# Optimization experiments

Measured on AMD Instinct MI355X. Metric: run time of the kernel, lower is better.

Reference implementation:

```python
import jax, jax.numpy as jnp
import numpy as np
import math

DIM = 96
D_MODEL = 2 * DIM
EXPAND = 2
D_INNER = EXPAND * D_MODEL  # 384
D_STATE = 16
D_CONV = 3
DT_RANK = math.ceil(D_MODEL / 16)  # 12
K = 4
B, H, W = 2, 56, 56


def setup_inputs() -> dict:
    key = jax.random.key(0)
    ks = jax.random.split(key, 10)
    s = lambda k, shp, sc=0.02: jax.random.normal(k, shp, jnp.float32) * sc
    inp = {}
    inp["x"] = jax.random.normal(ks[0], (B, DIM, H, W), jnp.float32)
    inp["conv_init_w"] = s(ks[1], (2 * DIM, DIM))
    inp["conv_init_b"] = jnp.zeros((2 * DIM,), jnp.float32)
    inp["in_proj_w"] = s(ks[2], (2 * D_INNER, D_MODEL))
    inp["conv2d_w"] = s(ks[3], (D_INNER, 1, D_CONV, D_CONV), 0.1)
    inp["conv2d_b"] = jnp.zeros((D_INNER,), jnp.float32)
    inp["x_proj_w"] = s(ks[4], (K, DT_RANK + 2 * D_STATE, D_INNER))
    inp["dt_proj_w"] = s(ks[5], (K, D_INNER, DT_RANK), 0.1)
    inp["dt_proj_b"] = s(ks[6], (K, D_INNER), 0.1)
    A = jnp.tile(jnp.arange(1, D_STATE + 1, dtype=jnp.float32), (K, D_INNER, 1))
    inp["A_log"] = jnp.log(A)  # (K, d_inner, d_state)
    inp["Ds"] = jnp.ones((K, D_INNER), jnp.float32)
    inp["ln_g"] = jnp.ones((D_INNER,), jnp.float32)
    inp["ln_b"] = jnp.zeros((D_INNER,), jnp.float32)
    inp["out_proj_w"] = s(ks[7], (D_MODEL, D_INNER))
    inp["conv_fina_w"] = s(ks[8], (DIM, 2 * DIM))
    inp["conv_fina_b"] = jnp.zeros((DIM,), jnp.float32)
    return inp


def _gelu(x):
    return jax.nn.gelu(x, approximate=False)


def _silu(x):
    return x * jax.nn.sigmoid(x)


def _selective_scan(u, delta, A, Bs, Cs, D):
    # u, delta: (b,K,d,L); A: (K,d,N); Bs,Cs: (b,K,N,L); D: (K,d)
    b, k, d, L = u.shape
    N = A.shape[-1]

    def step(hst, inp):
        u_t, dl_t, B_t, C_t = inp  # (b,K,d),(b,K,d),(b,K,N),(b,K,N)
        hst = jnp.exp(dl_t[..., None] * A) * hst + (dl_t * u_t)[..., None] * B_t[:, :, None, :]
        y = jnp.einsum('bkdn,bkn->bkd', hst, C_t)
        return hst, y

    seq = (jnp.moveaxis(u, -1, 0), jnp.moveaxis(delta, -1, 0),
           jnp.moveaxis(Bs, -1, 0), jnp.moveaxis(Cs, -1, 0))
    h0 = jnp.zeros((b, k, d, N), u.dtype)
    _, ys = jax.lax.scan(step, h0, seq)
    y = jnp.moveaxis(ys, 0, -1)  # (b,K,d,L)
    return y + u * D[None, :, :, None]


def reference(x, conv_init_w, conv_init_b, in_proj_w, conv2d_w, conv2d_b,
              x_proj_w, dt_proj_w, dt_proj_b, A_log, Ds, ln_g, ln_b,
              out_proj_w, conv_fina_w, conv_fina_b):
    b, c, h, w = x.shape
    # conv_init: 1x1 conv + GELU (dim -> 2*dim)
    x1 = _gelu(jnp.einsum('bchw,oc->bohw', x, conv_init_w) + conv_init_b[None, :, None, None])
    x0 = x1
    xh = jnp.transpose(x1, (0, 2, 3, 1))  # b h w c
    # --- SS2D ---
    xz = xh @ in_proj_w.T  # (b,h,w,2*d_inner)
    xi, z = jnp.split(xz, 2, axis=-1)
    xi = jnp.transpose(xi, (0, 3, 1, 2))  # b d h w
    xi = jax.lax.conv_general_dilated(xi, conv2d_w, (1, 1), 'SAME',
                                      dimension_numbers=('NCHW', 'OIHW', 'NCHW'),
                                      feature_group_count=xi.shape[1])
    xi = _silu(xi + conv2d_b[None, :, None, None])
    d = xi.shape[1]
    L = h * w
    x_flat = xi.reshape(b, d, L)
    x_tr = jnp.transpose(xi, (0, 1, 3, 2)).reshape(b, d, L)  # column-major scan
    xs = jnp.stack([x_flat, x_tr], axis=1)                   # (b,2,d,L)
    xs = jnp.concatenate([xs, jnp.flip(xs, axis=-1)], 1)     # (b,4,d,L)
    x_dbl = jnp.einsum('bkdl,kcd->bkcl', xs, x_proj_w)
    dts = x_dbl[:, :, :DT_RANK]
    Bs = x_dbl[:, :, DT_RANK:DT_RANK + D_STATE]
    Cs = x_dbl[:, :, DT_RANK + D_STATE:]
    dts = jnp.einsum('bkrl,kdr->bkdl', dts, dt_proj_w)
    delta = jax.nn.softplus(dts + dt_proj_b[None, :, :, None])
    A = -jnp.exp(A_log)  # (K,d,N)
    out_y = _selective_scan(xs, delta, A, Bs, Cs, Ds)  # (b,4,d,L)
    inv_y = jnp.flip(out_y[:, 2:4], axis=-1)
    y1 = out_y[:, 0]
    y2 = inv_y[:, 0]
    wb = lambda t: jnp.transpose(t.reshape(b, d, w, h), (0, 1, 3, 2)).reshape(b, d, L)
    y3 = wb(out_y[:, 1])
    y4 = wb(inv_y[:, 1])
    y = y1 + y2 + y3 + y4  # (b,d,L)
    y = jnp.transpose(y, (0, 2, 1)).reshape(b, h, w, d)
    mu = y.mean(-1, keepdims=True)
    var = ((y - mu) ** 2).mean(-1, keepdims=True)
    y = (y - mu) * jax.lax.rsqrt(var + 1e-5) * ln_g + ln_b
    y = y * _silu(z)
    y = y @ out_proj_w.T  # (b,h,w,d_model)
    y = jnp.transpose(y, (0, 3, 1, 2))  # b c h w
    # residual add with x0, then conv_fina 1x1 + GELU
    out = _gelu(jnp.einsum('bchw,oc->bohw', y + x0, conv_fina_w) + conv_fina_b[None, :, None, None])
    return out
```

## Files before the change

kernel.cpp:

```cpp
#include <hip/hip_runtime.h>


#define LPIX 3136
#define HH 56
#define SEG 32
#define SEGLEN 98

__device__ __forceinline__ float gelu_f(float x) {
    return 0.5f * x * (1.0f + erff(x * 0.70710678118654752f));
}

__device__ __forceinline__ float quad_sum(float p) {
    p += __int_as_float(__builtin_amdgcn_update_dpp(0, __float_as_int(p), 0xB1, 0xf, 0xf, true));
    p += __int_as_float(__builtin_amdgcn_update_dpp(0, __float_as_int(p), 0x4E, 0xf, 0xf, true));
    return p;
}

template <int MODE>
__global__ __launch_bounds__(256) void gemm_k(
    const float* __restrict__ A, const float* __restrict__ A2,
    const float* __restrict__ W, const float* __restrict__ bias,
    float* __restrict__ out0, float* __restrict__ out1,
    int M, int N, int Kd)
{
    __shared__ __align__(16) float As[32][68];
    __shared__ __align__(16) float Ws[32][68];
    const int tid = threadIdx.x;
    const int m0 = blockIdx.x * 64;
    const int n0 = blockIdx.y * 64;
    const int kz = blockIdx.z;
    const int mi = tid >> 4, ni = tid & 15;
    const float* Ause = A;
    if constexpr (MODE == 4) {
        if (kz & 1) Ause = A2;
        W += (size_t)kz * 44 * Kd;
    }
    float acc[4][4] = {};

    for (int k0 = 0; k0 < Kd; k0 += 32) {
        #pragma unroll
        for (int p = 0; p < 2; ++p) {
            int r = (tid >> 3) + p * 32;
            int kv = (tid & 7) * 4;
            int m = m0 + r;
            float4 v;
            if constexpr (MODE == 3) {
                int b = m / LPIX, l = m % LPIX;
                const float* px = Ause + ((size_t)(b * 96 + k0 + kv)) * LPIX + l;
                v.x = px[0]; v.y = px[LPIX]; v.z = px[2 * LPIX]; v.w = px[3 * LPIX];
            } else {
                v = *reinterpret_cast<const float4*>(Ause + (size_t)m * Kd + k0 + kv);
                if constexpr (MODE == 2) {
                    float4 r2 = *reinterpret_cast<const float4*>(A2 + (size_t)m * Kd + k0 + kv);
                    v.x += r2.x; v.y += r2.y; v.z += r2.z; v.w += r2.w;
                }
            }
            As[kv + 0][r] = v.x; As[kv + 1][r] = v.y;
            As[kv + 2][r] = v.z; As[kv + 3][r] = v.w;
        }
        #pragma unroll
        for (int p = 0; p < 2; ++p) {
            int r = (tid >> 3) + p * 32;
            int kv = (tid & 7) * 4;
            int n = n0 + r;
            float4 v = make_float4(0.f, 0.f, 0.f, 0.f);
            if (n < N) v = *reinterpret_cast<const float4*>(W + (size_t)n * Kd + k0 + kv);
            Ws[kv + 0][r] = v.x; Ws[kv + 1][r] = v.y;
            Ws[kv + 2][r] = v.z; Ws[kv + 3][r] = v.w;
        }
        __syncthreads();
        #pragma unroll
        for (int kk = 0; kk < 32; ++kk) {
            float4 a = *reinterpret_cast<const float4*>(&As[kk][mi * 4]);
            float4 b = *reinterpret_cast<const float4*>(&Ws[kk][ni * 4]);
            float av[4] = {a.x, a.y, a.z, a.w};
            float bv[4] = {b.x, b.y, b.z, b.w};
            #pragma unroll
            for (int i = 0; i < 4; ++i)
                #pragma unroll
                for (int j = 0; j < 4; ++j)
                    acc[i][j] = fmaf(av[i], bv[j], acc[i][j]);
        }
        __syncthreads();
    }

    #pragma unroll
    for (int i = 0; i < 4; ++i) {
        int m = m0 + mi * 4 + i;
        int b = m / LPIX, l = m % LPIX;
        #pragma unroll
        for (int j = 0; j < 4; ++j) {
            int o = n0 + ni * 4 + j;
            float v = acc[i][j];
            if constexpr (MODE == 0) {
                if (o < 384) out0[((size_t)(b * 384 + o)) * LPIX + l] = v;
                else         out1[(size_t)m * 384 + (o - 384)] = v;
            } else if constexpr (MODE == 1) {
                out0[(size_t)m * N + o] = v;
            } else if constexpr (MODE == 2) {
                if (o < N) out0[((size_t)(b * 96 + o)) * LPIX + l] = gelu_f(v + bias[o]);
            } else if constexpr (MODE == 3) {
                out0[(size_t)m * N + o] = gelu_f(v + bias[o]);
            } else {
                if (o < 44)
                    out0[(((size_t)b * 4 + kz) * LPIX + l) * 48 + o] = v;
            }
        }
    }
}

__global__ __launch_bounds__(256) void dwconv_k(
    const float* __restrict__ xin, const float* __restrict__ w9,
    const float* __restrict__ bias, float* __restrict__ xout)
{
    int f = blockIdx.x * 256 + threadIdx.x;
    if (f >= LPIX) return;
    int c = blockIdx.y, b = blockIdx.z;
    const float* p = xin + ((size_t)b * 384 + c) * LPIX;
    int h = f / HH, w = f % HH;
    float s = bias[c];
    #pragma unroll
    for (int dh = -1; dh <= 1; ++dh) {
        int h2 = h + dh;
        if ((unsigned)h2 >= HH) continue;
        #pragma unroll
        for (int dw = -1; dw <= 1; ++dw) {
            int w2 = w + dw;
            if ((unsigned)w2 >= HH) continue;
            s = fmaf(p[h2 * HH + w2], w9[c * 9 + (dh + 1) * 3 + (dw + 1)], s);
        }
    }
    xout[((size_t)b * 384 + c) * LPIX + f] = s / (1.f + __expf(-s));
}

__global__ __launch_bounds__(256) void transR_k(
    const float* __restrict__ xi, const float* __restrict__ Ds,
    float* __restrict__ xiR, float* __restrict__ y0)
{
    __shared__ float T[64][65];
    int f0 = blockIdx.x * 64, d0 = blockIdx.y * 64, b = blockIdx.z;
    int tid = threadIdx.x;
    #pragma unroll
    for (int i = 0; i < 16; ++i) {
        int idx = tid + i * 256;
        int dl = idx >> 6, fl = idx & 63;
        T[dl][fl] = xi[((size_t)b * 384 + d0 + dl) * LPIX + f0 + fl];
    }
    __syncthreads();
    #pragma unroll
    for (int i = 0; i < 16; ++i) {
        int idx = tid + i * 256;
        int fl = idx >> 6, dl = idx & 63;
        int d = d0 + dl;
        float v = T[dl][fl];
        float sD = Ds[d] + Ds[384 + d] + Ds[768 + d] + Ds[1152 + d];
        size_t o = ((size_t)b * LPIX + f0 + fl) * 384 + d;
        xiR[o] = v;
        y0[o] = v * sD;
    }
}

__global__ __launch_bounds__(256) void transT_k(
    const float* __restrict__ xi, float* __restrict__ xiT)
{
    __shared__ float T[64][57];
    int d0 = blockIdx.x * 64, h = blockIdx.y, b = blockIdx.z;
    int tid = threadIdx.x;
    #pragma unroll
    for (int i = 0; i < 14; ++i) {
        int idx = tid + i * 256;
        int dl = idx / 56, wl = idx % 56;
        T[dl][wl] = xi[((size_t)b * 384 + d0 + dl) * LPIX + h * 56 + wl];
    }
    __syncthreads();
    #pragma unroll
    for (int i = 0; i < 14; ++i) {
        int idx = tid + i * 256;
        int wl = idx >> 6, dl = idx & 63;
        xiT[((size_t)b * LPIX + wl * 56 + h) * 384 + d0 + dl] = T[dl][wl];
    }
}

__global__ __launch_bounds__(256) void dtgemm_k(
    const float* __restrict__ xdblT, const float* __restrict__ dtw,
    const float* __restrict__ dtb, float* __restrict__ dT)
{
    __shared__ float As[64][13];
    __shared__ float Ws[64][13];
    int t0 = blockIdx.x * 64, d0 = blockIdx.y * 64;
    int bk = blockIdx.z, k = bk & 3;
    int tid = threadIdx.x;
    const float* Ab = xdblT + ((size_t)bk * LPIX + t0) * 48;
    for (int i = tid; i < 768; i += 256) {
        int tt = i / 12, r = i % 12;
        As[tt][r] = Ab[(size_t)tt * 48 + r];
    }
    for (int i = tid; i < 768; i += 256) {
        int dd = i / 12, r = i % 12;
        Ws[dd][r] = dtw[((size_t)k * 384 + d0 + dd) * 12 + r];
    }
    __syncthreads();
    int mi = tid >> 4, ni = tid & 15;
    float acc[4][4] = {};
    #pragma unroll
    for (int r = 0; r < 12; ++r) {
        float av[4], bv[4];
        #pragma unroll
        for (int i = 0; i < 4; ++i) av[i] = As[mi * 4 + i][r];
        #pragma unroll
        for (int j = 0; j < 4; ++j) bv[j] = Ws[ni * 4 + j][r];
        #pragma unroll
        for (int i = 0; i < 4; ++i)
            #pragma unroll
            for (int j = 0; j < 4; ++j)
                acc[i][j] = fmaf(av[i], bv[j], acc[i][j]);
    }
    #pragma unroll
    for (int i = 0; i < 4; ++i) {
        int t = t0 + mi * 4 + i;
        #pragma unroll
        for (int j = 0; j < 4; ++j) {
            int d = d0 + ni * 4 + j;
            float s = acc[i][j] + dtb[k * 384 + d];
            s = (s > 20.f) ? s : log1pf(__expf(s));
            dT[((size_t)bk * LPIX + t) * 384 + d] = s;
        }
    }
}

__global__ __launch_bounds__(256) void scan1_k(
    const float* __restrict__ dT, const float* __restrict__ xiR,
    const float* __restrict__ xiT, const float* __restrict__ xdblT,
    const float* __restrict__ A_log, float* __restrict__ lh,
    float* __restrict__ sumd)
{
    int w = blockIdx.x * 4 + (threadIdx.x >> 6);
    int lane = threadIdx.x & 63;
    int dl_ = lane >> 2, nq = lane & 3;
    int seg = w & (SEG - 1);
    int dblk = (w >> 5) % 24;
    int bk = w / (SEG * 24);
    int b = bk >> 2, k = bk & 3;
    int d = dblk * 16 + dl_;

    float4 Ar = *reinterpret_cast<const float4*>(A_log + ((size_t)(k * 384 + d)) * 16 + nq * 4);
    float A2[4] = { -__expf(Ar.x) * 1.44269504f, -__expf(Ar.y) * 1.44269504f,
                    -__expf(Ar.z) * 1.44269504f, -__expf(Ar.w) * 1.44269504f };

    const float* pD = dT + (size_t)bk * LPIX * 384;
    const float* pU = ((k & 1) ? xiT : xiR) + (size_t)b * LPIX * 384;
    const float* pBC = xdblT + (size_t)bk * LPIX * 48;

    int t0 = seg * SEGLEN;
    int rev = k >> 1;
    int fpos0 = rev ? (LPIX - 1 - t0) : t0;
    int stepd = rev ? -384 : 384;
    int stepbc = rev ? -48 : 48;

    unsigned idx = (unsigned)fpos0 * 384u + (unsigned)d;
    unsigned ibc = (unsigned)fpos0 * 48u + 12u + (unsigned)nq * 4u;

    float h0 = 0.f, h1 = 0.f, h2 = 0.f, h3 = 0.f, sd = 0.f;

    float dlv = pD[idx], uv = pU[idx];
    float4 Bv = *reinterpret_cast<const float4*>(pBC + ibc);
    for (int s = 0; s < SEGLEN; ++s) {
        float dln, un; float4 Bn;
        if (s < SEGLEN - 1) {
            idx += stepd; ibc += stepbc;
            dln = pD[idx]; un = pU[idx];
            Bn = *reinterpret_cast<const float4*>(pBC + ibc);
        }
        sd += dlv;
        float dlu = dlv * uv;
        h0 = fmaf(__builtin_amdgcn_exp2f(dlv * A2[0]), h0, dlu * Bv.x);
        h1 = fmaf(__builtin_amdgcn_exp2f(dlv * A2[1]), h1, dlu * Bv.y);
        h2 = fmaf(__builtin_amdgcn_exp2f(dlv * A2[2]), h2, dlu * Bv.z);
        h3 = fmaf(__builtin_amdgcn_exp2f(dlv * A2[3]), h3, dlu * Bv.w);
        dlv = dln; uv = un; Bv = Bn;
    }
    size_t hb = (((size_t)seg * 8 + bk) * 384 + d) * 16 + nq * 4;
    *reinterpret_cast<float4*>(lh + hb) = make_float4(h0, h1, h2, h3);
    if (nq == 0)
        sumd[((size_t)seg * 8 + bk) * 384 + d] = sd;
}

__global__ __launch_bounds__(256) void scan2_k(
    float* __restrict__ lh, const float* __restrict__ sumd,
    const float* __restrict__ A_log)
{
    int idx = blockIdx.x * 256 + threadIdx.x;
    int n = idx & 15;
    int d = (idx >> 4) % 384;
    int bk = idx / (384 * 16);
    int k = bk & 3;
    float A2 = -__expf(A_log[((size_t)(k * 384 + d)) * 16 + n]) * 1.44269504f;
    float h = 0.f;
    for (int s = 0; s < SEG; ++s) {
        size_t base = (((size_t)s * 8 + bk) * 384 + d) * 16 + n;
        float lhv = lh[base];
        float P = __builtin_amdgcn_exp2f(sumd[((size_t)s * 8 + bk) * 384 + d] * A2);
        lh[base] = h;
        h = fmaf(P, h, lhv);
    }
}

template <int KK, int REV>
__device__ __forceinline__ void scan3_body(
    int b, int bk, int k, int seg, int d, int nq, int lane,
    const float* __restrict__ dT, const float* __restrict__ pU,
    const float* __restrict__ xdblT, const float* __restrict__ A_log,
    const float* __restrict__ lh, float* __restrict__ y0)
{
    float4 Ar = *reinterpret_cast<const float4*>(A_log + ((size_t)(k * 384 + d)) * 16 + nq * 4);
    float A2[4] = { -__expf(Ar.x) * 1.44269504f, -__expf(Ar.y) * 1.44269504f,
                    -__expf(Ar.z) * 1.44269504f, -__expf(Ar.w) * 1.44269504f };

    const float* pD = dT + (size_t)bk * LPIX * 384;
    const float* pBC = xdblT + (size_t)bk * LPIX * 48;
    float* pY = y0 + (size_t)b * LPIX * 384;

    int t0 = seg * SEGLEN;
    int fpos0 = REV ? (LPIX - 1 - t0) : t0;
    constexpr int stepd = REV ? -384 : 384;
    constexpr int stepbc = REV ? -48 : 48;

    unsigned idx = (unsigned)fpos0 * 384u + (unsigned)d;
    unsigned ibc = (unsigned)fpos0 * 48u + 12u + (unsigned)nq * 4u;

    unsigned iy; int rr;
    if constexpr (KK) {
        int r0 = fpos0 % 56, q0 = fpos0 / 56;
        rr = r0;
        iy = (unsigned)(r0 * 56 + q0) * 384u + (unsigned)d;
    } else {
        iy = idx;
        rr = 0; (void)rr;
    }

    size_t hb = (((size_t)seg * 8 + bk) * 384 + d) * 16 + nq * 4;
    float4 h4 = *reinterpret_cast<const float4*>(lh + hb);
    float h0 = h4.x, h1 = h4.y, h2 = h4.z, h3 = h4.w;

    float dlv = pD[idx], uv = pU[idx];
    float4 Bv = *reinterpret_cast<const float4*>(pBC + ibc);
    float4 Cv = *reinterpret_cast<const float4*>(pBC + ibc + 16);

    for (int s = 0; s < SEGLEN; ++s) {
        float dln, un; float4 Bn, Cn;
        if (s < SEGLEN - 1) {
            idx += stepd; ibc += stepbc;
            dln = pD[idx]; un = pU[idx];
            Bn = *reinterpret_cast<const float4*>(pBC + ibc);
            Cn = *reinterpret_cast<const float4*>(pBC + ibc + 16);
        }
        float dlu = dlv * uv;
        h0 = fmaf(__builtin_amdgcn_exp2f(dlv * A2[0]), h0, dlu * Bv.x);
        float p = h0 * Cv.x;
        h1 = fmaf(__builtin_amdgcn_exp2f(dlv * A2[1]), h1, dlu * Bv.y);
        p = fmaf(h1, Cv.y, p);
        h2 = fmaf(__builtin_amdgcn_exp2f(dlv * A2[2]), h2, dlu * Bv.z);
        p = fmaf(h2, Cv.z, p);
        h3 = fmaf(__builtin_amdgcn_exp2f(dlv * A2[3]), h3, dlu * Bv.w);
        p = fmaf(h3, Cv.w, p);
        p = quad_sum(p);
        if ((lane & 3) == 0)
            __hip_atomic_fetch_add(pY + iy, p,
                                   __ATOMIC_RELAXED, __HIP_MEMORY_SCOPE_AGENT);
        if constexpr (KK) {
            if constexpr (REV) {
                bool wrap = (rr == 0);
                iy += wrap ? (unsigned)(3079 * 384) : (unsigned)(-56 * 384);
                rr = wrap ? 55 : rr - 1;
            } else {
                bool wrap = (rr == 55);
                iy += wrap ? (unsigned)(-3079 * 384) : (unsigned)(56 * 384);
                rr = wrap ? 0 : rr + 1;
            }
        } else {
            iy += (unsigned)stepd;
        }
        dlv = dln; uv = un; Bv = Bn; Cv = Cn;
    }
}

__global__ __launch_bounds__(256) void scan3_k(
    const float* __restrict__ dT, const float* __restrict__ xiR,
    const float* __restrict__ xiT, const float* __restrict__ xdblT,
    const float* __restrict__ A_log, const float* __restrict__ lh,
    float* __restrict__ y0)
{
    int w = blockIdx.x * 4 + (threadIdx.x >> 6);
    int lane = threadIdx.x & 63;
    int dl_ = lane >> 2, nq = lane & 3;
    int seg = w & (SEG - 1);
    int dblk = (w >> 5) % 24;
    int bk = w / (SEG * 24);
    int b = bk >> 2, k = bk & 3;
    int d = dblk * 16 + dl_;
    const float* pU = ((k & 1) ? xiT : xiR) + (size_t)b * LPIX * 384;
    if (k == 0)      scan3_body<0, 0>(b, bk, k, seg, d, nq, lane, dT, pU, xdblT, A_log, lh, y0);
    else if (k == 1) scan3_body<1, 0>(b, bk, k, seg, d, nq, lane, dT, pU, xdblT, A_log, lh, y0);
    else if (k == 2) scan3_body<0, 1>(b, bk, k, seg, d, nq, lane, dT, pU, xdblT, A_log, lh, y0);
    else             scan3_body<1, 1>(b, bk, k, seg, d, nq, lane, dT, pU, xdblT, A_log, lh, y0);
}

__global__ __launch_bounds__(256) void lngate_k(
    const float* __restrict__ y0, const float* __restrict__ z,
    const float* __restrict__ lng, const float* __restrict__ lnb,
    float* __restrict__ gbuf)
{
    int m = blockIdx.x * 4 + (threadIdx.x >> 6);
    int lane = threadIdx.x & 63;
    const float* py = y0 + (size_t)m * 384;
    float v[6];
    float s = 0.f, sq = 0.f;
    #pragma unroll
    for (int i = 0; i < 6; ++i) {
        v[i] = py[lane + i * 64];
        s += v[i]; sq += v[i] * v[i];
    }
    #pragma unroll
    for (int off = 1; off < 64; off <<= 1) {
        s += __shfl_xor(s, off);
        sq += __shfl_xor(sq, off);
    }
    float mu = s * (1.f / 384.f);
    float var = sq * (1.f / 384.f) - mu * mu;
    float rs = rsqrtf(var + 1e-5f);
    const float* pz = z + (size_t)m * 384;
    float* pg = gbuf + (size_t)m * 384;
    #pragma unroll
    for (int i = 0; i < 6; ++i) {
        int c = lane + i * 64;
        float nv = (v[i] - mu) * rs * lng[c] + lnb[c];
        float zv = pz[c];
        pg[c] = nv * (zv / (1.f + __expf(-zv)));
    }
}

extern "C" void kernel_launch(void* const* d_in, const int* in_sizes, int n_in,
                              void* d_out, int out_size, void* d_ws, size_t ws_size,
                              hipStream_t stream) {
    const float* x        = (const float*)d_in[0];
    const float* w_init   = (const float*)d_in[1];
    const float* b_init   = (const float*)d_in[2];
    const float* w_inproj = (const float*)d_in[3];
    const float* w_conv   = (const float*)d_in[4];
    const float* b_conv   = (const float*)d_in[5];
    const float* w_xproj  = (const float*)d_in[6];
    const float* w_dt     = (const float*)d_in[7];
    const float* b_dt     = (const float*)d_in[8];
    const float* A_log    = (const float*)d_in[9];
    const float* Ds       = (const float*)d_in[10];
    const float* ln_g     = (const float*)d_in[11];
    const float* ln_b     = (const float*)d_in[12];
    const float* w_out    = (const float*)d_in[13];
    const float* w_fina   = (const float*)d_in[14];
    const float* b_fina   = (const float*)d_in[15];

    float* ws    = (float*)d_ws;
    float* x1    = ws + 0;
    float* z     = ws + 1204224;
    float* xiR   = ws + 3612672;
    float* xiT   = ws + 6021120;
    float* xdblT = ws + 8429568;
    float* dT    = ws + 9633792;
    float* xiraw = ws + 9633792;
    float* xi    = ws + 12042240;
    float* y0    = ws + 19267584;
    float* lh    = ws + 21676032;
    float* sumd  = ws + 23248896;
    float* out   = (float*)d_out;

    gemm_k<3><<<dim3(98, 3), 256, 0, stream>>>(x, nullptr, w_init, b_init,
                                               x1, nullptr, 6272, 192, 96);
    gemm_k<0><<<dim3(98, 12), 256, 0, stream>>>(x1, nullptr, w_inproj, nullptr,
                                                xiraw, z, 6272, 768, 192);
    dwconv_k<<<dim3(13, 384, 2), 256, 0, stream>>>(xiraw, w_conv, b_conv, xi);
    transR_k<<<dim3(49, 6, 2), 256, 0, stream>>>(xi, Ds, xiR, y0);
    transT_k<<<dim3(6, 56, 2), 256, 0, stream>>>(xi, xiT);
    gemm_k<4><<<dim3(98, 1, 4), 256, 0, stream>>>(xiR, xiT, w_xproj, nullptr,
                                                  xdblT, nullptr, 6272, 44, 384);
    dtgemm_k<<<dim3(49, 6, 8), 256, 0, stream>>>(xdblT, w_dt, b_dt, dT);
    scan1_k<<<1536, 256, 0, stream>>>(dT, xiR, xiT, xdblT, A_log, lh, sumd);
    scan2_k<<<192, 256, 0, stream>>>(lh, sumd, A_log);
    scan3_k<<<1536, 256, 0, stream>>>(dT, xiR, xiT, xdblT, A_log, lh, y0);
    lngate_k<<<1568, 256, 0, stream>>>(y0, z, ln_g, ln_b, xiR);
    gemm_k<1><<<dim3(98, 3), 256, 0, stream>>>(xiR, nullptr, w_out, nullptr,
                                               dT, nullptr, 6272, 192, 384);
    gemm_k<2><<<dim3(98, 2), 256, 0, stream>>>(dT, x1, w_fina, b_fina,
                                               out, nullptr, 6272, 96, 192);
}
```

Before: 399.7 us.

## Fuse dwconv with transposes, add 128-row GEMM tiles, rebalance scan segments

The depthwise conv + SiLU now reads the channel-last in_proj output straight from a shared-memory tile and writes xiR, xiT and the D-skip term in one pass, replacing three kernels (dwconv, transR, transT). The in_proj, x_proj and out_proj GEMMs move to a 128-row tile variant with vectorised row-major stores, and the init GEMM loads its channel-major input with vector loads. The scan now uses 49 segments of 64 steps instead of 32 of 98, which gives more parallel blocks at the cost of a longer serial carry pass in scan2. The workspace layout is reshuffled so buffers can alias.

```diff
diff --git a/kernel.cpp b/kernel.cpp
--- a/kernel.cpp
+++ b/kernel.cpp
@@ -3,8 +3,9 @@
 
 #define LPIX 3136
 #define HH 56
-#define SEG 32
-#define SEGLEN 98
+#define SEG 49
+#define SEGLEN 64
+#define LOG2E 1.44269504f
 
 __device__ __forceinline__ float gelu_f(float x) {
     return 0.5f * x * (1.0f + erff(x * 0.70710678118654752f));
@@ -16,47 +17,38 @@
     return p;
 }
 
-template <int MODE>
+template <int AM, int EM>
 __global__ __launch_bounds__(256) void gemm_k(
     const float* __restrict__ A, const float* __restrict__ A2,
     const float* __restrict__ W, const float* __restrict__ bias,
-    float* __restrict__ out0, float* __restrict__ out1,
-    int M, int N, int Kd)
+    float* __restrict__ out0, int M, int N, int Kd)
 {
     __shared__ __align__(16) float As[32][68];
     __shared__ __align__(16) float Ws[32][68];
     const int tid = threadIdx.x;
     const int m0 = blockIdx.x * 64;
     const int n0 = blockIdx.y * 64;
-    const int kz = blockIdx.z;
     const int mi = tid >> 4, ni = tid & 15;
-    const float* Ause = A;
-    if constexpr (MODE == 4) {
-        if (kz & 1) Ause = A2;
-        W += (size_t)kz * 44 * Kd;
-    }
+    const int bI = m0 / LPIX, l0 = m0 % LPIX;
     float acc[4][4] = {};
 
     for (int k0 = 0; k0 < Kd; k0 += 32) {
-        #pragma unroll
-        for (int p = 0; p < 2; ++p) {
-            int r = (tid >> 3) + p * 32;
-            int kv = (tid & 7) * 4;
-            int m = m0 + r;
-            float4 v;
-            if constexpr (MODE == 3) {
-                int b = m / LPIX, l = m % LPIX;
-                const float* px = Ause + ((size_t)(b * 96 + k0 + kv)) * LPIX + l;
-                v.x = px[0]; v.y = px[LPIX]; v.z = px[2 * LPIX]; v.w = px[3 * LPIX];
-            } else {
-                v = *reinterpret_cast<const float4*>(Ause + (size_t)m * Kd + k0 + kv);
-                if constexpr (MODE == 2) {
-                    float4 r2 = *reinterpret_cast<const float4*>(A2 + (size_t)m * Kd + k0 + kv);
-                    v.x += r2.x; v.y += r2.y; v.z += r2.z; v.w += r2.w;
-                }
+        if constexpr (AM == 1) {
+            int kr = tid >> 3, ms = (tid & 7) * 8;
+            const float* pa = A + ((size_t)(bI * 96 + k0 + kr)) * LPIX + l0 + ms;
+            *(float4*)&As[kr][ms] = *(const float4*)pa;
+            *(float4*)&As[kr][ms + 4] = *(const float4*)(pa + 4);
+        } else {
+            #pragma unroll
+            for (int p = 0; p < 2; ++p) {
+                int r = (tid >> 3) + p * 32;
+                int kv = (tid & 7) * 4;
+                float4 v = *(const float4*)(A + (size_t)(m0 + r) * Kd + k0 + kv);
+                float4 w2 = *(const float4*)(A2 + (size_t)(m0 + r) * Kd + k0 + kv);
+                v.x += w2.x; v.y += w2.y; v.z += w2.z; v.w += w2.w;
+                As[kv + 0][r] = v.x; As[kv + 1][r] = v.y;
+                As[kv + 2][r] = v.z; As[kv + 3][r] = v.w;
             }
-            As[kv + 0][r] = v.x; As[kv + 1][r] = v.y;
-            As[kv + 2][r] = v.z; As[kv + 3][r] = v.w;
         }
         #pragma unroll
         for (int p = 0; p < 2; ++p) {
@@ -64,15 +56,15 @@
             int kv = (tid & 7) * 4;
             int n = n0 + r;
             float4 v = make_float4(0.f, 0.f, 0.f, 0.f);
-            if (n < N) v = *reinterpret_cast<const float4*>(W + (size_t)n * Kd + k0 + kv);
+            if (n < N) v = *(const float4*)(W + (size_t)n * Kd + k0 + kv);
             Ws[kv + 0][r] = v.x; Ws[kv + 1][r] = v.y;
             Ws[kv + 2][r] = v.z; Ws[kv + 3][r] = v.w;
         }
         __syncthreads();
         #pragma unroll
         for (int kk = 0; kk < 32; ++kk) {
-            float4 a = *reinterpret_cast<const float4*>(&As[kk][mi * 4]);
-            float4 b = *reinterpret_cast<const float4*>(&Ws[kk][ni * 4]);
+            float4 a = *(const float4*)&As[kk][mi * 4];
+            float4 b = *(const float4*)&Ws[kk][ni * 4];
             float av[4] = {a.x, a.y, a.z, a.w};
             float bv[4] = {b.x, b.y, b.z, b.w};
             #pragma unroll
@@ -87,97 +79,159 @@
     #pragma unroll
     for (int i = 0; i < 4; ++i) {
         int m = m0 + mi * 4 + i;
-        int b = m / LPIX, l = m % LPIX;
-        #pragma unroll
-        for (int j = 0; j < 4; ++j) {
-            int o = n0 + ni * 4 + j;
-            float v = acc[i][j];
-            if constexpr (MODE == 0) {
-                if (o < 384) out0[((size_t)(b * 384 + o)) * LPIX + l] = v;
-                else         out1[(size_t)m * 384 + (o - 384)] = v;
-            } else if constexpr (MODE == 1) {
-                out0[(size_t)m * N + o] = v;
-            } else if constexpr (MODE == 2) {
-                if (o < N) out0[((size_t)(b * 96 + o)) * LPIX + l] = gelu_f(v + bias[o]);
-            } else if constexpr (MODE == 3) {
-                out0[(size_t)m * N + o] = gelu_f(v + bias[o]);
-            } else {
+        int l = l0 + mi * 4 + i;
+        int o0 = n0 + ni * 4;
+        if constexpr (EM == 3) {
+            #pragma unroll
+            for (int j = 0; j < 4; ++j) {
+                int o = o0 + j;
+                if (o < N)
+                    out0[((size_t)(bI * 96 + o)) * LPIX + l] = gelu_f(acc[i][j] + bias[o]);
+            }
+        } else {
+            float4 g;
+            g.x = gelu_f(acc[i][0] + bias[o0 + 0]);
+            g.y = gelu_f(acc[i][1] + bias[o0 + 1]);
+            g.z = gelu_f(acc[i][2] + bias[o0 + 2]);
+            g.w = gelu_f(acc[i][3] + bias[o0 + 3]);
+            *(float4*)&out0[(size_t)m * N + o0] = g;
+        }
+        (void)m;
+    }
+}
+
+template <int EM>
+__global__ __launch_bounds__(256) void gemm128_k(
+    const float* __restrict__ A, const float* __restrict__ A2,
+    const float* __restrict__ W,
+    float* __restrict__ out0, float* __restrict__ out1,
+    int M, int N, int Kd)
+{
+    __shared__ __align__(16) float As[32][132];
+    __shared__ __align__(16) float Ws[32][68];
+    const int tid = threadIdx.x;
+    const int m0 = blockIdx.x * 128;
+    const int n0 = blockIdx.y * 64;
+    const int kz = blockIdx.z;
+    const int mi = tid >> 4, ni = tid & 15;
+    const float* Ap = A;
+    const float* Wp = W;
+    if constexpr (EM == 2) {
+        if (kz & 1) Ap = A2;
+        Wp += (size_t)kz * 44 * Kd;
+    }
+    float acc[8][4] = {};
+
+    for (int k0 = 0; k0 < Kd; k0 += 32) {
+        #pragma unroll
+        for (int p = 0; p < 4; ++p) {
+            int r = (tid >> 3) + p * 32;
+            int kv = (tid & 7) * 4;
+            float4 v = *(const float4*)(Ap + (size_t)(m0 + r) * Kd + k0 + kv);
+            As[kv + 0][r] = v.x; As[kv + 1][r] = v.y;
+            As[kv + 2][r] = v.z; As[kv + 3][r] = v.w;
+        }
+        #pragma unroll
+        for (int p = 0; p < 2; ++p) {
+            int r = (tid >> 3) + p * 32;
+            int kv = (tid & 7) * 4;
+            int n = n0 + r;
+            float4 v = make_float4(0.f, 0.f, 0.f, 0.f);
+            if (n < N) v = *(const float4*)(Wp + (size_t)n * Kd + k0 + kv);
+            Ws[kv + 0][r] = v.x; Ws[kv + 1][r] = v.y;
+            Ws[kv + 2][r] = v.z; Ws[kv + 3][r] = v.w;
+        }
+        __syncthreads();
+        #pragma unroll
+        for (int kk = 0; kk < 32; ++kk) {
+            float4 a0 = *(const float4*)&As[kk][mi * 8];
+            float4 a1 = *(const float4*)&As[kk][mi * 8 + 4];
+            float4 b  = *(const float4*)&Ws[kk][ni * 4];
+            float av[8] = {a0.x, a0.y, a0.z, a0.w, a1.x, a1.y, a1.z, a1.w};
+            float bv[4] = {b.x, b.y, b.z, b.w};
+            #pragma unroll
+            for (int i = 0; i < 8; ++i)
+                #pragma unroll
+                for (int j = 0; j < 4; ++j)
+                    acc[i][j] = fmaf(av[i], bv[j], acc[i][j]);
+        }
+        __syncthreads();
+    }
+
+    #pragma unroll
+    for (int i = 0; i < 8; ++i) {
+        int m = m0 + mi * 8 + i;
+        int o0 = n0 + ni * 4;
+        if constexpr (EM == 0) {
+            *(float4*)&out0[(size_t)m * N + o0] =
+                make_float4(acc[i][0], acc[i][1], acc[i][2], acc[i][3]);
+        } else if constexpr (EM == 1) {
+            float4 v = make_float4(acc[i][0], acc[i][1], acc[i][2], acc[i][3]);
+            if (o0 < 384) *(float4*)&out0[(size_t)m * 384 + o0] = v;
+            else          *(float4*)&out1[(size_t)m * 384 + (o0 - 384)] = v;
+        } else {
+            int bI = m / LPIX, l = m - bI * LPIX;
+            #pragma unroll
+            for (int j = 0; j < 4; ++j) {
+                int o = o0 + j;
                 if (o < 44)
-                    out0[(((size_t)b * 4 + kz) * LPIX + l) * 48 + o] = v;
+                    out0[(((size_t)bI * 4 + kz) * LPIX + l) * 48 + o] = acc[i][j];
             }
         }
     }
 }
 
-__global__ __launch_bounds__(256) void dwconv_k(
-    const float* __restrict__ xin, const float* __restrict__ w9,
-    const float* __restrict__ bias, float* __restrict__ xout)
-{
-    int f = blockIdx.x * 256 + threadIdx.x;
-    if (f >= LPIX) return;
-    int c = blockIdx.y, b = blockIdx.z;
-    const float* p = xin + ((size_t)b * 384 + c) * LPIX;
-    int h = f / HH, w = f % HH;
-    float s = bias[c];
-    #pragma unroll
-    for (int dh = -1; dh <= 1; ++dh) {
-        int h2 = h + dh;
-        if ((unsigned)h2 >= HH) continue;
-        #pragma unroll
-        for (int dw = -1; dw <= 1; ++dw) {
-            int w2 = w + dw;
-            if ((unsigned)w2 >= HH) continue;
-            s = fmaf(p[h2 * HH + w2], w9[c * 9 + (dh + 1) * 3 + (dw + 1)], s);
-        }
-    }
-    xout[((size_t)b * 384 + c) * LPIX + f] = s / (1.f + __expf(-s));
-}
-
-__global__ __launch_bounds__(256) void transR_k(
-    const float* __restrict__ xi, const float* __restrict__ Ds,
-    float* __restrict__ xiR, float* __restrict__ y0)
-{
-    __shared__ float T[64][65];
-    int f0 = blockIdx.x * 64, d0 = blockIdx.y * 64, b = blockIdx.z;
-    int tid = threadIdx.x;
-    #pragma unroll
-    for (int i = 0; i < 16; ++i) {
-        int idx = tid + i * 256;
-        int dl = idx >> 6, fl = idx & 63;
-        T[dl][fl] = xi[((size_t)b * 384 + d0 + dl) * LPIX + f0 + fl];
+__global__ __launch_bounds__(256) void dwsilu_k(
+    const float* __restrict__ xs, const float* __restrict__ w9,
+    const float* __restrict__ cb, const float* __restrict__ Ds,
+    float* __restrict__ xiR, float* __restrict__ xiT, float* __restrict__ y0)
+{
+    __shared__ float S[32][339];
+    const int h0 = blockIdx.x * 4;
+    const int d0 = blockIdx.y * 32;
+    const int b  = blockIdx.z;
+    const int tid = threadIdx.x;
+    const int fbase = h0 * HH - HH;
+    if (tid < 32) { S[tid][0] = 0.f; S[tid][337] = 0.f; S[tid][338] = 0.f; }
+    for (int it = tid; it < 336 * 8; it += 256) {
+        int cc = it >> 3, q = it & 7;
+        int f = fbase + cc;
+        float4 v = make_float4(0.f, 0.f, 0.f, 0.f);
+        if ((unsigned)f < LPIX)
+            v = *(const float4*)(xs + ((size_t)b * LPIX + f) * 384 + d0 + q * 4);
+        S[q * 4 + 0][cc + 1] = v.x; S[q * 4 + 1][cc + 1] = v.y;
+        S[q * 4 + 2][cc + 1] = v.z; S[q * 4 + 3][cc + 1] = v.w;
     }
     __syncthreads();
-    #pragma unroll
-    for (int i = 0; i < 16; ++i) {
-        int idx = tid + i * 256;
-        int fl = idx >> 6, dl = idx & 63;
-        int d = d0 + dl;
-        float v = T[dl][fl];
-        float sD = Ds[d] + Ds[384 + d] + Ds[768 + d] + Ds[1152 + d];
-        size_t o = ((size_t)b * LPIX + f0 + fl) * 384 + d;
+    const int dl = tid & 31, fc = tid >> 5;
+    const int d = d0 + dl;
+    float wr[9];
+    #pragma unroll
+    for (int t = 0; t < 9; ++t) wr[t] = w9[d * 9 + t];
+    const float bs = cb[d];
+    const float sD = Ds[d] + Ds[384 + d] + Ds[768 + d] + Ds[1152 + d];
+    const int hh = h0 + (fc >> 1);
+    const int w0 = (fc & 1) * 28;
+    for (int j = 0; j < 28; ++j) {
+        int fl = fc * 28 + j;
+        int f = h0 * HH + fl;
+        int c = fl + 57;
+        int w = w0 + j;
+        float ml = (w > 0) ? 1.f : 0.f;
+        float mr = (w < 55) ? 1.f : 0.f;
+        float s = bs;
+        #pragma unroll
+        for (int tr = 0; tr < 3; ++tr) {
+            int cc = c + (tr - 1) * 56;
+            s = fmaf(S[dl][cc - 1], wr[tr * 3 + 0] * ml, s);
+            s = fmaf(S[dl][cc],     wr[tr * 3 + 1], s);
+            s = fmaf(S[dl][cc + 1], wr[tr * 3 + 2] * mr, s);
+        }
+        float v = s / (1.f + __expf(-s));
+        size_t o = ((size_t)b * LPIX + f) * 384 + d;
         xiR[o] = v;
         y0[o] = v * sD;
-    }
-}
-
-__global__ __launch_bounds__(256) void transT_k(
-    const float* __restrict__ xi, float* __restrict__ xiT)
-{
-    __shared__ float T[64][57];
-    int d0 = blockIdx.x * 64, h = blockIdx.y, b = blockIdx.z;
-    int tid = threadIdx.x;
-    #pragma unroll
-    for (int i = 0; i < 14; ++i) {
-        int idx = tid + i * 256;
-        int dl = idx / 56, wl = idx % 56;
-        T[dl][wl] = xi[((size_t)b * 384 + d0 + dl) * LPIX + h * 56 + wl];
-    }
-    __syncthreads();
-    #pragma unroll
-    for (int i = 0; i < 14; ++i) {
-        int idx = tid + i * 256;
-        int wl = idx >> 6, dl = idx & 63;
-        xiT[((size_t)b * LPIX + wl * 56 + h) * 384 + d0 + dl] = T[dl][wl];
+        xiT[((size_t)b * LPIX + (w * HH + hh)) * 384 + d] = v;
     }
 }
 
@@ -237,15 +291,16 @@
     int w = blockIdx.x * 4 + (threadIdx.x >> 6);
     int lane = threadIdx.x & 63;
     int dl_ = lane >> 2, nq = lane & 3;
-    int seg = w & (SEG - 1);
-    int dblk = (w >> 5) % 24;
-    int bk = w / (SEG * 24);
+    int seg = w % SEG;
+    int chain = w / SEG;
+    int dblk = chain % 24;
+    int bk = chain / 24;
     int b = bk >> 2, k = bk & 3;
     int d = dblk * 16 + dl_;
 
     float4 Ar = *reinterpret_cast<const float4*>(A_log + ((size_t)(k * 384 + d)) * 16 + nq * 4);
-    float A2[4] = { -__expf(Ar.x) * 1.44269504f, -__expf(Ar.y) * 1.44269504f,
-                    -__expf(Ar.z) * 1.44269504f, -__expf(Ar.w) * 1.44269504f };
+    float A2[4] = { -__expf(Ar.x) * LOG2E, -__expf(Ar.y) * LOG2E,
+                    -__expf(Ar.z) * LOG2E, -__expf(Ar.w) * LOG2E };
 
     const float* pD = dT + (size_t)bk * LPIX * 384;
     const float* pU = ((k & 1) ? xiT : xiR) + (size_t)b * LPIX * 384;
@@ -294,7 +349,7 @@
     int d = (idx >> 4) % 384;
     int bk = idx / (384 * 16);
     int k = bk & 3;
-    float A2 = -__expf(A_log[((size_t)(k * 384 + d)) * 16 + n]) * 1.44269504f;
+    float A2 = -__expf(A_log[((size_t)(k * 384 + d)) * 16 + n]) * LOG2E;
     float h = 0.f;
     for (int s = 0; s < SEG; ++s) {
         size_t base = (((size_t)s * 8 + bk) * 384 + d) * 16 + n;
@@ -313,8 +368,8 @@
     const float* __restrict__ lh, float* __restrict__ y0)
 {
     float4 Ar = *reinterpret_cast<const float4*>(A_log + ((size_t)(k * 384 + d)) * 16 + nq * 4);
-    float A2[4] = { -__expf(Ar.x) * 1.44269504f, -__expf(Ar.y) * 1.44269504f,
-                    -__expf(Ar.z) * 1.44269504f, -__expf(Ar.w) * 1.44269504f };
+    float A2[4] = { -__expf(Ar.x) * LOG2E, -__expf(Ar.y) * LOG2E,
+                    -__expf(Ar.z) * LOG2E, -__expf(Ar.w) * LOG2E };
 
     const float* pD = dT + (size_t)bk * LPIX * 384;
     const float* pBC = xdblT + (size_t)bk * LPIX * 48;
@@ -393,9 +448,10 @@
     int w = blockIdx.x * 4 + (threadIdx.x >> 6);
     int lane = threadIdx.x & 63;
     int dl_ = lane >> 2, nq = lane & 3;
-    int seg = w & (SEG - 1);
-    int dblk = (w >> 5) % 24;
-    int bk = w / (SEG * 24);
+    int seg = w % SEG;
+    int chain = w / SEG;
+    int dblk = chain % 24;
+    int bk = chain / 24;
     int b = bk >> 2, k = bk & 3;
     int d = dblk * 16 + dl_;
     const float* pU = ((k & 1) ? xiT : xiR) + (size_t)b * LPIX * 384;
@@ -432,10 +488,10 @@
     float* pg = gbuf + (size_t)m * 384;
     #pragma unroll
     for (int i = 0; i < 6; ++i) {
-        int c = lane + i * 64;
-        float nv = (v[i] - mu) * rs * lng[c] + lnb[c];
-        float zv = pz[c];
-        pg[c] = nv * (zv / (1.f + __expf(-zv)));
+        int ch = lane + i * 64;
+        float nv = (v[i] - mu) * rs * lng[ch] + lnb[ch];
+        float zv = pz[ch];
+        pg[ch] = nv * (zv / (1.f + __expf(-zv)));
     }
 }
 
@@ -461,34 +517,32 @@
 
     float* ws    = (float*)d_ws;
     float* x1    = ws + 0;
-    float* z     = ws + 1204224;
-    float* xiR   = ws + 3612672;
-    float* xiT   = ws + 6021120;
-    float* xdblT = ws + 8429568;
-    float* dT    = ws + 9633792;
-    float* xiraw = ws + 9633792;
-    float* xi    = ws + 12042240;
-    float* y0    = ws + 19267584;
-    float* lh    = ws + 21676032;
-    float* sumd  = ws + 23248896;
+    float* xis   = ws + 1204224;
+    float* lh    = ws + 1204224;
+    float* z     = ws + 3612672;
+    float* xiR   = ws + 6021120;
+    float* xiT   = ws + 8429568;
+    float* xdblT = ws + 10838016;
+    float* dT    = ws + 12042240;
+    float* y0    = ws + 21676032;
+    float* sumd  = ws + 24084480;
     float* out   = (float*)d_out;
 
-    gemm_k<3><<<dim3(98, 3), 256, 0, stream>>>(x, nullptr, w_init, b_init,
-                                               x1, nullptr, 6272, 192, 96);
-    gemm_k<0><<<dim3(98, 12), 256, 0, stream>>>(x1, nullptr, w_inproj, nullptr,
-                                                xiraw, z, 6272, 768, 192);
-    dwconv_k<<<dim3(13, 384, 2), 256, 0, stream>>>(xiraw, w_conv, b_conv, xi);
-    transR_k<<<dim3(49, 6, 2), 256, 0, stream>>>(xi, Ds, xiR, y0);
-    transT_k<<<dim3(6, 56, 2), 256, 0, stream>>>(xi, xiT);
-    gemm_k<4><<<dim3(98, 1, 4), 256, 0, stream>>>(xiR, xiT, w_xproj, nullptr,
-                                                  xdblT, nullptr, 6272, 44, 384);
+    gemm_k<1, 4><<<dim3(98, 3), 256, 0, stream>>>(x, nullptr, w_init, b_init,
+                                                  x1, 6272, 192, 96);
+    gemm128_k<1><<<dim3(49, 12), 256, 0, stream>>>(x1, nullptr, w_inproj,
+                                                   xis, z, 6272, 768, 192);
+    dwsilu_k<<<dim3(14, 12, 2), 256, 0, stream>>>(xis, w_conv, b_conv, Ds,
+                                                  xiR, xiT, y0);
+    gemm128_k<2><<<dim3(49, 1, 4), 256, 0, stream>>>(xiR, xiT, w_xproj,
+                                                     xdblT, nullptr, 6272, 44, 384);
     dtgemm_k<<<dim3(49, 6, 8), 256, 0, stream>>>(xdblT, w_dt, b_dt, dT);
-    scan1_k<<<1536, 256, 0, stream>>>(dT, xiR, xiT, xdblT, A_log, lh, sumd);
+    scan1_k<<<2352, 256, 0, stream>>>(dT, xiR, xiT, xdblT, A_log, lh, sumd);
     scan2_k<<<192, 256, 0, stream>>>(lh, sumd, A_log);
-    scan3_k<<<1536, 256, 0, stream>>>(dT, xiR, xiT, xdblT, A_log, lh, y0);
+    scan3_k<<<2352, 256, 0, stream>>>(dT, xiR, xiT, xdblT, A_log, lh, y0);
     lngate_k<<<1568, 256, 0, stream>>>(y0, z, ln_g, ln_b, xiR);
-    gemm_k<1><<<dim3(98, 3), 256, 0, stream>>>(xiR, nullptr, w_out, nullptr,
-                                               dT, nullptr, 6272, 192, 384);
-    gemm_k<2><<<dim3(98, 2), 256, 0, stream>>>(dT, x1, w_fina, b_fina,
-                                               out, nullptr, 6272, 96, 192);
-}
+    gemm128_k<0><<<dim3(49, 3), 256, 0, stream>>>(xiR, nullptr, w_out,
+                                                  xiT, nullptr, 6272, 192, 384);
+    gemm_k<2, 3><<<dim3(98, 2), 256, 0, stream>>>(xiT, x1, w_fina, b_fina,
+                                                  out, 6272, 96, 192);
+}
```

New measurement: 402.6 us. No clear change (+0.7%).
